# Optimization experiments

Measured on AMD Instinct MI355X. Metric: run time of the kernel, lower is better.

Reference implementation:

```python
import jax, jax.numpy as jnp
import numpy as np

N, C, T = 8, 256, 512
H, KQ, OUT = 8, 256, 256
EPS = 1e-5


def sym_linear(x, w, stride):
    # w: (2, out_dim); circulant-grouped expansion to (2T, out_dim), then x @ cp
    out_dim = w.shape[1]
    idx = (jnp.arange(out_dim)[None, :] - jnp.arange(T)[:, None] * stride) % out_dim  # (T, out_dim)
    cp = w[:, idx].transpose(1, 0, 2).reshape(2 * T, out_dim)  # cat of rolled copies
    return x @ cp


def ln2d(x, g, b):
    # LayerNorm over last two dims (T, 2T) with affine params (T, 2T)
    mu = jnp.mean(x, axis=(-2, -1), keepdims=True)
    var = jnp.mean(jnp.square(x - mu), axis=(-2, -1), keepdims=True)
    return (x - mu) / jnp.sqrt(var + EPS) * g + b


def setup_inputs() -> dict:
    key = jax.random.key(0)
    ks = jax.random.split(key, 16)
    stdv = 1.0 / np.sqrt(2 * T)
    u = lambda k, shape, s: jax.random.uniform(k, shape, jnp.float32, -s, s)
    return {
        "x": jax.random.normal(ks[0], (N, C, T), jnp.float32),
        "Wq": u(ks[1], (KQ, C), 1.0 / np.sqrt(C)),
        "Wk": u(ks[2], (KQ, C), 1.0 / np.sqrt(C)),
        "Wv": u(ks[3], (OUT, C), 1.0 / np.sqrt(C)),
        "m1w0": u(ks[4], (2, 2 * T), stdv),
        "m2w0": u(ks[5], (2, 2 * T), stdv),
        "m1w1": u(ks[6], (2, 2 * T), stdv),
        "m2w1": u(ks[7], (2, T), stdv),
        "ln1g0": 1.0 + 0.1 * jax.random.normal(ks[8], (T, 2 * T), jnp.float32),
        "ln1b0": 0.1 * jax.random.normal(ks[9], (T, 2 * T), jnp.float32),
        "ln2g0": 1.0 + 0.1 * jax.random.normal(ks[10], (T, 2 * T), jnp.float32),
        "ln2b0": 0.1 * jax.random.normal(ks[11], (T, 2 * T), jnp.float32),
        "ln1g1": 1.0 + 0.1 * jax.random.normal(ks[12], (T, 2 * T), jnp.float32),
        "ln1b1": 0.1 * jax.random.normal(ks[13], (T, 2 * T), jnp.float32),
    }


def reference(x, Wq, Wk, Wv, m1w0, m2w0, m1w1, m2w1,
              ln1g0, ln1b0, ln2g0, ln2b0, ln1g1, ln1b1):
    dk = KQ // H
    q = jnp.einsum('oc,nct->not', Wq, x).reshape(N, H, dk, T).transpose(0, 1, 3, 2)  # (N,H,T,dk)
    k = jnp.einsum('oc,nct->not', Wk, x).reshape(N, H, dk, T)                        # (N,H,dk,T)
    v = jnp.einsum('oc,nct->not', Wv, x).reshape(N, H, OUT // H, T).transpose(0, 1, 3, 2)  # (N,H,T,dv)

    scores = jnp.einsum('nhtd,nhds->nhts', q, k) / np.sqrt(dk)  # (N,H,T,T)
    ar = jnp.arange(T, dtype=jnp.float32)
    pd = jnp.abs(ar[None, :] - ar[:, None]) / (T - 1)  # (T,T)
    p = jnp.stack([scores, jnp.broadcast_to(pd, scores.shape)], axis=-1)  # (N,H,T,T,2)
    p = p.reshape(N, H, T, 2 * T)

    def transpose_pairs(z):
        return z.reshape(N, H, T, T, 2).transpose(0, 1, 3, 2, 4)

    # mix block 0 (intermediate)
    p = ln2d(sym_linear(p, m1w0, 2), ln1g0, ln1b0)
    p = jax.nn.gelu(transpose_pairs(p), approximate=False).reshape(N, H, T, 2 * T)
    p = ln2d(sym_linear(p, m2w0, 2), ln2g0, ln2b0)
    p = jax.nn.gelu(transpose_pairs(p), approximate=False).reshape(N, H, T, 2 * T)

    # mix block 1 (final)
    p = ln2d(sym_linear(p, m1w1, 2), ln1g1, ln1b1)
    p = jax.nn.gelu(transpose_pairs(p), approximate=False).reshape(N, H, T, 2 * T)
    p = sym_linear(p, m2w1, 1)           # (N,H,T,T), out_roll_stride = T // T * 1
    p = p.transpose(0, 1, 3, 2)

    attn = jax.nn.softmax(p, axis=-1)
    out = jnp.einsum('nhts,nhsd->nhtd', attn, v)  # (N,H,T,dv)
    return out.transpose(0, 1, 3, 2).reshape(N, OUT, T)
```

## Files before the change

### kernel.cpp

```cpp
#include <hip/hip_runtime.h>
#include <hip/hip_bf16.h>
#include <math.h>

#define CDIM 256
#define TDIM 512
#define T2   1024
#define NB   64
#define MTOT 524288.0f

typedef __bf16 bf16x8 __attribute__((ext_vector_type(8)));
typedef float  f32x4  __attribute__((ext_vector_type(4)));

__device__ __forceinline__ ushort f2bf(float f) {
  union { float f; unsigned u; } v; v.f = f;
  unsigned r = v.u + 0x7fffu + ((v.u >> 16) & 1u);
  return (ushort)(r >> 16);
}
__device__ __forceinline__ float bf2f(ushort h) {
  union { unsigned u; float f; } v; v.u = ((unsigned)h) << 16;
  return v.f;
}
__device__ __forceinline__ float gelu_exact(float x) {
  return 0.5f * x * (1.0f + erff(x * 0.7071067811865475f));
}

#define TO_LDS(p)  ((__attribute__((address_space(3))) void*)(unsigned)(uintptr_t)(p))
#define TO_GLB(p)  ((const __attribute__((address_space(1))) void*)(uintptr_t)(p))
#define GLOAD_LDS16(g, l) __builtin_amdgcn_global_load_lds(TO_GLB(g), TO_LDS(l), 16, 0, 0)

#define BAR()    asm volatile("s_barrier" ::: "memory")
#define WAITL()  asm volatile("s_waitcnt lgkmcnt(0)" ::: "memory")
#define WAITV4() asm volatile("s_waitcnt vmcnt(4)" ::: "memory")
#define WAITV0() asm volatile("s_waitcnt vmcnt(0)" ::: "memory")

__global__ __launch_bounds__(256)
void proj_kernel(const float* __restrict__ x, const float* __restrict__ Wq,
                 const float* __restrict__ Wk, const float* __restrict__ Wv,
                 ushort* __restrict__ qb, ushort* __restrict__ kb,
                 float* __restrict__ vp) {
  int t = blockIdx.x * 256 + threadIdx.x;
  int o = blockIdx.y;
  int n = blockIdx.z;
  const float* xn = x + (long)n * CDIM * TDIM;
  float aq = 0.f, ak = 0.f, av = 0.f;
  for (int c = 0; c < CDIM; ++c) {
    float xv = xn[c * TDIM + t];
    aq = fmaf(Wq[o * CDIM + c], xv, aq);
    ak = fmaf(Wk[o * CDIM + c], xv, ak);
    av = fmaf(Wv[o * CDIM + c], xv, av);
  }
  int h = o >> 5, d = o & 31;
  long bidx = (((long)(n * 8 + h) * 512) + t) * 32 + d;
  qb[bidx] = f2bf(aq);
  kb[bidx] = f2bf(ak);
  vp[((long)n * 256 + o) * TDIM + t] = av;
}

__global__ __launch_bounds__(256)
void prep_kernel(const float* __restrict__ m1w0, const float* __restrict__ m2w0,
                 const float* __restrict__ m1w1, const float* __restrict__ m2w1,
                 ushort* __restrict__ cpte0, ushort* __restrict__ cpto0,
                 ushort* __restrict__ cpt1, ushort* __restrict__ cpt2,
                 ushort* __restrict__ cpt3, ushort* __restrict__ pdb) {
  long i = (long)blockIdx.x * 256 + threadIdx.x;
  if (i < 524288) {
    int o = (int)(i >> 9), s = (int)(i & 511);
    int idx = (o - 2 * s) & 1023;
    cpte0[i] = f2bf(m1w0[idx]);
    cpto0[i] = f2bf(m1w0[1024 + idx]);
  } else if (i < 1572864) {
    long j = i - 524288;
    int o = (int)(j >> 10), kk = (int)(j & 1023);
    cpt1[j] = f2bf(m2w0[(kk & 1) * 1024 + ((o - 2 * (kk >> 1)) & 1023)]);
  } else if (i < 2621440) {
    long j = i - 1572864;
    int o = (int)(j >> 10), kk = (int)(j & 1023);
    cpt2[j] = f2bf(m1w1[(kk & 1) * 1024 + ((o - 2 * (kk >> 1)) & 1023)]);
  } else if (i < 3145728) {
    long j = i - 2621440;
    int o = (int)(j >> 10), kk = (int)(j & 1023);
    cpt3[j] = f2bf(m2w1[(kk & 1) * 512 + ((o - (kk >> 1)) & 511)]);
  } else if (i < 3407872) {
    long j = i - 3145728;
    int t = (int)(j >> 9), s = (int)(j & 511);
    pdb[j] = f2bf(fabsf((float)(s - t)) * (1.0f / 511.0f));
  }
}

__global__ __launch_bounds__(256)
void scores_kernel(const ushort* __restrict__ qb, const ushort* __restrict__ kb,
                   ushort* __restrict__ S) {
  int tb = blockIdx.x;
  int b  = blockIdx.y;
  int wv = threadIdx.x >> 6, lane = threadIdx.x & 63;
  int fr = lane & 15, fq = lane >> 4;
  int t0 = tb * 64 + wv * 16;
  bf16x8 af = *(const bf16x8*)(qb + ((long)b * 512 + t0 + fr) * 32 + fq * 8);
  const ushort* kbase = kb + (long)b * 512 * 32 + fr * 32 + fq * 8;
  ushort* Sb = S + ((long)b * 512 + t0 + fq * 4) * 512 + fr;
  f32x4 zz = {0.f, 0.f, 0.f, 0.f};
#pragma unroll 4
  for (int st = 0; st < 32; ++st) {
    bf16x8 bfv = *(const bf16x8*)(kbase + st * 512);
    f32x4 acc = __builtin_amdgcn_mfma_f32_16x16x32_bf16(af, bfv, zz, 0, 0, 0);
#pragma unroll
    for (int r = 0; r < 4; ++r)
      Sb[(long)r * 512 + st * 16] = f2bf(acc[r] * 0.17677669529663687f);
  }
}

#define LDS_BUF  65536
#define LDS_BOFF 32768

#define STAGE_A_(buf, h, kt) do { \
  const ushort* gA0_ = Ab + (long)((h)*128 +      sr0) * K + (kt)*64 + slog8; \
  const ushort* gA1_ = Ab + (long)((h)*128 + 64 + sr0) * K + (kt)*64 + slog8; \
  char* dA_ = ldsw + (size_t)(buf) * LDS_BUF + (h)*16384 + tid*16; \
  GLOAD_LDS16(gA0_, dA_); GLOAD_LDS16(gA1_, dA_ + 8192); } while(0)

#define STAGE_B_(buf, h, kt) do { \
  const ushort* gB0_ = Bb + (long)((h)*128 +      sr0) * K + (kt)*64 + slog8; \
  const ushort* gB1_ = Bb + (long)((h)*128 + 64 + sr0) * K + (kt)*64 + slog8; \
  char* dB_ = ldsw + (size_t)(buf) * LDS_BUF + LDS_BOFF + (h)*16384 + tid*16; \
  GLOAD_LDS16(gB0_, dB_); GLOAD_LDS16(gB1_, dB_ + 8192); } while(0)

#define LD_A_(buf, mh) do { \
  const char* aB_ = ldsc + (size_t)(buf) * LDS_BUF; \
  _Pragma("unroll") for (int mi = 0; mi < 4; ++mi) { \
    int ar_ = wm*128 + (mh)*64 + mi*16 + fr; \
    const char* rb_ = aB_ + ar_*128; int sw_ = (ar_&7)<<4; \
    af[mi][0] = *(const bf16x8*)(rb_ + ((fq*16) ^ sw_)); \
    af[mi][1] = *(const bf16x8*)(rb_ + ((64 + fq*16) ^ sw_)); \
  } } while(0)

#define LD_B_(dst, buf, nh) do { \
  const char* bB_ = ldsc + (size_t)(buf) * LDS_BUF + LDS_BOFF; \
  _Pragma("unroll") for (int ni = 0; ni < 2; ++ni) { \
    int br_ = wn*64 + (nh)*32 + ni*16 + fr; \
    const char* rb_ = bB_ + br_*128; int sw_ = (br_&7)<<4; \
    dst[ni][0] = *(const bf16x8*)(rb_ + ((fq*16) ^ sw_)); \
    dst[ni][1] = *(const bf16x8*)(rb_ + ((64 + fq*16) ^ sw_)); \
  } } while(0)

#define QUAD_(mh, nh, bfa) do { \
  __builtin_amdgcn_s_setprio(1); \
  _Pragma("unroll") for (int kk = 0; kk < 2; ++kk) \
  _Pragma("unroll") for (int mi = 0; mi < 4; ++mi) \
  _Pragma("unroll") for (int ni = 0; ni < 2; ++ni) \
    acc[(mh)*4+mi][(nh)*2+ni] = __builtin_amdgcn_mfma_f32_16x16x32_bf16( \
        af[mi][kk], bfa[ni][kk], acc[(mh)*4+mi][(nh)*2+ni], 0, 0, 0); \
  __builtin_amdgcn_s_setprio(0); } while(0)

template<int K, bool FINAL>
__global__ __launch_bounds__(512, 2)
void gemm256_kernel(const ushort* __restrict__ A, long aStride,
                    const ushort* __restrict__ BT, long bStride,
                    void* __restrict__ Out, int ncols, float* __restrict__ stats,
                    const float* __restrict__ Cadd) {
  __shared__ ushort lds[2][2][256 * 64];
  const int tid = threadIdx.x;
  const int bm = blockIdx.x, bn = blockIdx.y, b = blockIdx.z;
  constexpr int NKT2 = K >> 7;
  const ushort* Ab = A  + (long)b * aStride + (long)bm * 256 * K;
  const ushort* Bb = BT + (long)b * bStride + (long)bn * 256 * K;
  const int lane = tid & 63;
  const int fr = lane & 15, fq = lane >> 4;
  const int wid = tid >> 6, wm = wid >> 2, wn = wid & 3;
  const int sr0 = tid >> 3;
  const int slog8 = ((tid & 7) ^ (sr0 & 7)) * 8;
  const char* ldsc = (const char*)&lds[0][0][0];
  char*       ldsw = (char*)&lds[0][0][0];

  f32x4 acc[8][4] = {};
  bf16x8 af[4][2], bf0[2][2], bf1[2][2];

  STAGE_B_(0, 0, 0); STAGE_B_(0, 1, 0);
  STAGE_A_(0, 0, 0); STAGE_A_(0, 1, 0);
  STAGE_B_(1, 0, 1); STAGE_B_(1, 1, 1);
  WAITV4();
  BAR();

  for (int i = 0; i < NKT2; ++i) {
    const int t1 = 2 * i + 1, t2 = 2 * i + 2, t3 = 2 * i + 3;
    const bool st = (i < NKT2 - 1);
    LD_A_(0, 0); LD_B_(bf0, 0, 0);
    STAGE_A_(1, 0, t1);
    BAR(); WAITL(); QUAD_(0, 0, bf0); BAR();

    LD_B_(bf1, 0, 1);
    STAGE_A_(1, 1, t1);
    BAR(); WAITL(); QUAD_(0, 1, bf1); BAR();

    LD_A_(0, 1);
    if (st) STAGE_B_(0, 0, t2);
    BAR(); WAITL(); QUAD_(1, 1, bf1); BAR();

    if (st) { STAGE_B_(0, 1, t2); WAITV4(); } else { WAITV0(); }
    BAR(); QUAD_(1, 0, bf0); BAR();

    LD_A_(1, 0); LD_B_(bf0, 1, 0);
    if (st) STAGE_A_(0, 0, t2);
    BAR(); WAITL(); QUAD_(0, 0, bf0); BAR();

    LD_B_(bf1, 1, 1);
    if (st) STAGE_A_(0, 1, t2);
    BAR(); WAITL(); QUAD_(0, 1, bf1); BAR();

    LD_A_(1, 1);
    if (st) STAGE_B_(1, 0, t3);
    BAR(); WAITL(); QUAD_(1, 1, bf1); BAR();

    if (st) { STAGE_B_(1, 1, t3); WAITV4(); }
    BAR(); QUAD_(1, 0, bf0); BAR();
  }

  const int r0 = bm * 256 + wm * 128;
  const int c0 = bn * 256 + wn * 64;
  if (!FINAL) {
    ushort* Yb = (ushort*)Out + (long)b * 512 * ncols;
    float s1 = 0.f, s2 = 0.f;
#pragma unroll
    for (int mi = 0; mi < 8; ++mi)
#pragma unroll
      for (int ni = 0; ni < 4; ++ni)
#pragma unroll
        for (int r = 0; r < 4; ++r) {
          float v = acc[mi][ni][r];
          int row = r0 + mi * 16 + fq * 4 + r;
          int col = c0 + ni * 16 + fr;
          if (Cadd) v += Cadd[(long)row * ncols + col];
          s1 += v; s2 += v * v;
          Yb[(long)row * ncols + col] = f2bf(v);
        }
    __syncthreads();
    float* red = (float*)&lds[0][0][0];
    red[tid] = s1; red[tid + 512] = s2;
    __syncthreads();
    for (int off = 256; off > 0; off >>= 1) {
      if (tid < off) { red[tid] += red[tid + off]; red[512 + tid] += red[512 + tid + off]; }
      __syncthreads();
    }
    if (tid == 0) {
      atomicAdd(&stats[b * 2],     red[0]);
      atomicAdd(&stats[b * 2 + 1], red[512]);
    }
  } else {
    float* Lb = (float*)Out + (long)b * 512 * ncols;
#pragma unroll
    for (int mi = 0; mi < 8; ++mi)
#pragma unroll
      for (int ni = 0; ni < 4; ++ni)
#pragma unroll
        for (int r = 0; r < 4; ++r) {
          int row = r0 + mi * 16 + fq * 4 + r;
          int col = c0 + ni * 16 + fr;
          Lb[(long)row * ncols + col] = acc[mi][ni][r];
        }
  }
}

__global__ __launch_bounds__(256)
void apply_kernel(const ushort* __restrict__ Y, const float* __restrict__ stats,
                  const float* __restrict__ g, const float* __restrict__ bia,
                  ushort* __restrict__ P) {
  __shared__ ushort2 tile[32][33];
  int ti = blockIdx.x;
  int si = blockIdx.y;
  int b  = blockIdx.z;
  float mu  = stats[b * 2] * (1.0f / MTOT);
  float var = stats[b * 2 + 1] * (1.0f / MTOT) - mu * mu;
  float rstd = rsqrtf(var + 1e-5f);
  int tx = threadIdx.x & 31, ty = threadIdx.x >> 5;
  const ushort* Yb = Y + (long)b * 512 * 1024;
#pragma unroll
  for (int i = 0; i < 4; ++i) {
    int t  = ti * 32 + ty + i * 8;
    int sp = si * 32 + tx;
    ushort2 yv = *(const ushort2*)(Yb + (long)t * 1024 + 2 * sp);
    float2 gv = *(const float2*)(g   + (long)t * 1024 + 2 * sp);
    float2 bv = *(const float2*)(bia + (long)t * 1024 + 2 * sp);
    float y0 = (bf2f(yv.x) - mu) * rstd * gv.x + bv.x;
    float y1 = (bf2f(yv.y) - mu) * rstd * gv.y + bv.y;
    ushort2 o; o.x = f2bf(gelu_exact(y0)); o.y = f2bf(gelu_exact(y1));
    tile[ty + i * 8][tx] = o;
  }
  __syncthreads();
  ushort* Pb = P + (long)b * 512 * 1024;
#pragma unroll
  for (int i = 0; i < 4; ++i) {
    int srow = si * 32 + ty + i * 8;
    int tcol = ti * 32 + tx;
    ushort2 v = tile[tx][ty + i * 8];
    *(ushort2*)(Pb + (long)srow * 1024 + 2 * tcol) = v;
  }
}

__global__ __launch_bounds__(256)
void smax_av_kernel(const float* __restrict__ L, const float* __restrict__ vp,
                    float* __restrict__ out) {
  __shared__ float Lt[32][513];
  int bh = blockIdx.x;
  int at = blockIdx.y;
  int n = bh >> 3, h = bh & 7;
  int wv = threadIdx.x >> 6, lane = threadIdx.x & 63;
  for (int rr = 0; rr < 8; ++rr) {
    int row = wv * 8 + rr;
    int a = at * 32 + row;
    const float* Lr = L + ((long)bh * 512 + a) * 512;
    float e[8];
#pragma unroll
    for (int j = 0; j < 8; ++j) e[j] = Lr[j * 64 + lane];
    float m = e[0];
#pragma unroll
    for (int j = 1; j < 8; ++j) m = fmaxf(m, e[j]);
    for (int off = 32; off > 0; off >>= 1) m = fmaxf(m, __shfl_xor(m, off, 64));
    float s = 0.f;
#pragma unroll
    for (int j = 0; j < 8; ++j) { e[j] = expf(e[j] - m); s += e[j]; }
    for (int off = 32; off > 0; off >>= 1) s += __shfl_xor(s, off, 64);
    float inv = 1.0f / s;
#pragma unroll
    for (int j = 0; j < 8; ++j) Lt[row][j * 64 + lane] = e[j] * inv;
  }
  __syncthreads();
  int r  = threadIdx.x & 31;
  int d0 = (threadIdx.x >> 5) * 4;
  const float* vb = vp + ((long)n * 256 + h * 32) * 512;
  float a0 = 0.f, a1 = 0.f, a2 = 0.f, a3 = 0.f;
  for (int bc = 0; bc < 512; bc += 4) {
    float4 v0 = *(const float4*)(vb + (d0 + 0) * 512 + bc);
    float4 v1 = *(const float4*)(vb + (d0 + 1) * 512 + bc);
    float4 v2 = *(const float4*)(vb + (d0 + 2) * 512 + bc);
    float4 v3 = *(const float4*)(vb + (d0 + 3) * 512 + bc);
    float p0 = Lt[r][bc], p1 = Lt[r][bc + 1], p2 = Lt[r][bc + 2], p3 = Lt[r][bc + 3];
    a0 = fmaf(p0, v0.x, fmaf(p1, v0.y, fmaf(p2, v0.z, fmaf(p3, v0.w, a0))));
    a1 = fmaf(p0, v1.x, fmaf(p1, v1.y, fmaf(p2, v1.z, fmaf(p3, v1.w, a1))));
    a2 = fmaf(p0, v2.x, fmaf(p1, v2.y, fmaf(p2, v2.z, fmaf(p3, v2.w, a2))));
    a3 = fmaf(p0, v3.x, fmaf(p1, v3.y, fmaf(p2, v3.z, fmaf(p3, v3.w, a3))));
  }
  int a = at * 32 + r;
  float* ob = out + ((long)n * 256 + h * 32) * 512;
  ob[(d0 + 0) * 512 + a] = a0;
  ob[(d0 + 1) * 512 + a] = a1;
  ob[(d0 + 2) * 512 + a] = a2;
  ob[(d0 + 3) * 512 + a] = a3;
}

extern "C" void kernel_launch(void* const* d_in, const int* in_sizes, int n_in,
                              void* d_out, int out_size, void* d_ws, size_t ws_size,
                              hipStream_t stream) {
  const float* x     = (const float*)d_in[0];
  const float* Wq    = (const float*)d_in[1];
  const float* Wk    = (const float*)d_in[2];
  const float* Wv    = (const float*)d_in[3];
  const float* m1w0  = (const float*)d_in[4];
  const float* m2w0  = (const float*)d_in[5];
  const float* m1w1  = (const float*)d_in[6];
  const float* m2w1  = (const float*)d_in[7];
  const float* ln1g0 = (const float*)d_in[8];
  const float* ln1b0 = (const float*)d_in[9];
  const float* ln2g0 = (const float*)d_in[10];
  const float* ln2b0 = (const float*)d_in[11];
  const float* ln1g1 = (const float*)d_in[12];
  const float* ln1b1 = (const float*)d_in[13];

  char* w = (char*)d_ws;
  float*  vp     = (float*) (w + 0);
  ushort* qb     = (ushort*)(w + (4ull  << 20));
  ushort* kb     = (ushort*)(w + (6ull  << 20));
  float*  stats  = (float*) (w + (8ull  << 20));
  ushort* cpte0  = (ushort*)(w + (9ull  << 20));
  ushort* cpto0  = (ushort*)(w + (10ull << 20));
  ushort* cpt1   = (ushort*)(w + (11ull << 20));
  ushort* cpt2   = (ushort*)(w + (13ull << 20));
  ushort* cpt3   = (ushort*)(w + (15ull << 20));
  ushort* pdb    = (ushort*)(w + (16ull << 20));
  float*  pdpart = (float*) (w + (17ull << 20));
  ushort* bufA   = (ushort*)(w + (20ull << 20));
  ushort* bufB   = (ushort*)(w + (84ull << 20));
  ushort* S      = bufA;
  float*  L      = (float*)bufB;
  float*  outp   = (float*)d_out;

  hipMemsetAsync(stats, 0, 3 * NB * 2 * sizeof(float), stream);

  proj_kernel<<<dim3(2, 256, 8), 256, 0, stream>>>(x, Wq, Wk, Wv, qb, kb, vp);
  prep_kernel<<<13312, 256, 0, stream>>>(m1w0, m2w0, m1w1, m2w1,
                                         cpte0, cpto0, cpt1, cpt2, cpt3, pdb);
  scores_kernel<<<dim3(8, 64), 256, 0, stream>>>(qb, kb, S);
  gemm256_kernel<512, true><<<dim3(2, 4, 1), 512, 0, stream>>>(
      pdb, 0, cpto0, 0, pdpart, 1024, nullptr, nullptr);
  gemm256_kernel<512, false><<<dim3(2, 4, 64), 512, 0, stream>>>(
      S, 512L * 512, cpte0, 0, bufB, 1024, stats, pdpart);
  apply_kernel<<<dim3(16, 16, 64), 256, 0, stream>>>(bufB, stats, ln1g0, ln1b0, bufA);
  gemm256_kernel<1024, false><<<dim3(2, 4, 64), 512, 0, stream>>>(
      bufA, 512L * 1024, cpt1, 0, bufB, 1024, stats + 128, nullptr);
  apply_kernel<<<dim3(16, 16, 64), 256, 0, stream>>>(bufB, stats + 128, ln2g0, ln2b0, bufA);
  gemm256_kernel<1024, false><<<dim3(2, 4, 64), 512, 0, stream>>>(
      bufA, 512L * 1024, cpt2, 0, bufB, 1024, stats + 256, nullptr);
  apply_kernel<<<dim3(16, 16, 64), 256, 0, stream>>>(bufB, stats + 256, ln1g1, ln1b1, bufA);
  gemm256_kernel<1024, true><<<dim3(2, 2, 64), 512, 0, stream>>>(
      cpt3, 0, bufA, 512L * 1024, L, 512, nullptr, nullptr);
  smax_av_kernel<<<dim3(64, 16), 256, 0, stream>>>(L, vp, outp);
}
```

Before: 516.3 us.

## Pack LayerNorm affine params to bf16, widen apply loads, merge GEMM barrier phases

Adds a prep kernel that converts the three LayerNorm gamma/beta sets to interleaved bf16, reusing the qb, kb and cpte0 workspace regions after they are consumed. The apply kernel now covers a 32x64 tile with 8-element vector loads and 16-byte transposed stores, cutting fp32 parameter traffic and raising access width. The GEMM main loop merges pairs of quads under one barrier pair, halving barriers per k-step. Rounding gamma and beta to bf16 adds a small precision loss, and the buffer reuse relies on the qb, kb and cpte0 data no longer being needed.

```diff
diff --git a/kernel.cpp b/kernel.cpp
--- a/kernel.cpp
+++ b/kernel.cpp
@@ -10,6 +10,8 @@
 
 typedef __bf16 bf16x8 __attribute__((ext_vector_type(8)));
 typedef float  f32x4  __attribute__((ext_vector_type(4)));
+typedef ushort ushort8v __attribute__((ext_vector_type(8)));
+typedef ushort ushort4v __attribute__((ext_vector_type(4)));
 
 __device__ __forceinline__ ushort f2bf(float f) {
   union { float f; unsigned u; } v; v.f = f;
@@ -88,6 +90,24 @@
 }
 
 __global__ __launch_bounds__(256)
+void prep2_kernel(const float* __restrict__ g0, const float* __restrict__ b0,
+                  const float* __restrict__ g1, const float* __restrict__ b1,
+                  const float* __restrict__ g2, const float* __restrict__ b2,
+                  ushort* __restrict__ gbb0, ushort* __restrict__ gbb1,
+                  ushort* __restrict__ gbb2) {
+  long i = (long)blockIdx.x * 256 + threadIdx.x;
+  int set = (int)(i >> 18);
+  long j = i & 262143;
+  const float* g = set == 0 ? g0 : (set == 1 ? g1 : g2);
+  const float* b = set == 0 ? b0 : (set == 1 ? b1 : b2);
+  ushort* gbb    = set == 0 ? gbb0 : (set == 1 ? gbb1 : gbb2);
+  float2 gv = *(const float2*)(g + 2 * j);
+  float2 bv = *(const float2*)(b + 2 * j);
+  ushort4v o; o[0] = f2bf(gv.x); o[1] = f2bf(bv.x); o[2] = f2bf(gv.y); o[3] = f2bf(bv.y);
+  *(ushort4v*)(gbb + 4 * j) = o;
+}
+
+__global__ __launch_bounds__(256)
 void scores_kernel(const ushort* __restrict__ qb, const ushort* __restrict__ kb,
                    ushort* __restrict__ S) {
   int tb = blockIdx.x;
@@ -183,35 +203,26 @@
   for (int i = 0; i < NKT2; ++i) {
     const int t1 = 2 * i + 1, t2 = 2 * i + 2, t3 = 2 * i + 3;
     const bool st = (i < NKT2 - 1);
-    LD_A_(0, 0); LD_B_(bf0, 0, 0);
-    STAGE_A_(1, 0, t1);
-    BAR(); WAITL(); QUAD_(0, 0, bf0); BAR();
-
-    LD_B_(bf1, 0, 1);
-    STAGE_A_(1, 1, t1);
-    BAR(); WAITL(); QUAD_(0, 1, bf1); BAR();
-
+    LD_A_(0, 0); LD_B_(bf0, 0, 0); LD_B_(bf1, 0, 1);
+    STAGE_A_(1, 0, t1); STAGE_A_(1, 1, t1);
+    BAR(); WAITL();
+    QUAD_(0, 0, bf0); QUAD_(0, 1, bf1);
+    BAR();
     LD_A_(0, 1);
-    if (st) STAGE_B_(0, 0, t2);
-    BAR(); WAITL(); QUAD_(1, 1, bf1); BAR();
-
-    if (st) { STAGE_B_(0, 1, t2); WAITV4(); } else { WAITV0(); }
-    BAR(); QUAD_(1, 0, bf0); BAR();
-
-    LD_A_(1, 0); LD_B_(bf0, 1, 0);
-    if (st) STAGE_A_(0, 0, t2);
-    BAR(); WAITL(); QUAD_(0, 0, bf0); BAR();
-
-    LD_B_(bf1, 1, 1);
-    if (st) STAGE_A_(0, 1, t2);
-    BAR(); WAITL(); QUAD_(0, 1, bf1); BAR();
-
+    if (st) { STAGE_B_(0, 0, t2); STAGE_B_(0, 1, t2); WAITV4(); } else { WAITV0(); }
+    BAR(); WAITL();
+    QUAD_(1, 1, bf1); QUAD_(1, 0, bf0);
+    BAR();
+    LD_A_(1, 0); LD_B_(bf0, 1, 0); LD_B_(bf1, 1, 1);
+    if (st) { STAGE_A_(0, 0, t2); STAGE_A_(0, 1, t2); }
+    BAR(); WAITL();
+    QUAD_(0, 0, bf0); QUAD_(0, 1, bf1);
+    BAR();
     LD_A_(1, 1);
-    if (st) STAGE_B_(1, 0, t3);
-    BAR(); WAITL(); QUAD_(1, 1, bf1); BAR();
-
-    if (st) { STAGE_B_(1, 1, t3); WAITV4(); }
-    BAR(); QUAD_(1, 0, bf0); BAR();
+    if (st) { STAGE_B_(1, 0, t3); STAGE_B_(1, 1, t3); WAITV4(); }
+    BAR(); WAITL();
+    QUAD_(1, 1, bf1); QUAD_(1, 0, bf0);
+    BAR();
   }
 
   const int r0 = bm * 256 + wm * 128;
@@ -261,37 +272,52 @@
 
 __global__ __launch_bounds__(256)
 void apply_kernel(const ushort* __restrict__ Y, const float* __restrict__ stats,
-                  const float* __restrict__ g, const float* __restrict__ bia,
-                  ushort* __restrict__ P) {
-  __shared__ ushort2 tile[32][33];
+                  const ushort* __restrict__ gbb, ushort* __restrict__ P) {
+  __shared__ ushort2 tile[32][65];
   int ti = blockIdx.x;
   int si = blockIdx.y;
   int b  = blockIdx.z;
   float mu  = stats[b * 2] * (1.0f / MTOT);
   float var = stats[b * 2 + 1] * (1.0f / MTOT) - mu * mu;
   float rstd = rsqrtf(var + 1e-5f);
-  int tx = threadIdx.x & 31, ty = threadIdx.x >> 5;
   const ushort* Yb = Y + (long)b * 512 * 1024;
-#pragma unroll
-  for (int i = 0; i < 4; ++i) {
-    int t  = ti * 32 + ty + i * 8;
-    int sp = si * 32 + tx;
-    ushort2 yv = *(const ushort2*)(Yb + (long)t * 1024 + 2 * sp);
-    float2 gv = *(const float2*)(g   + (long)t * 1024 + 2 * sp);
-    float2 bv = *(const float2*)(bia + (long)t * 1024 + 2 * sp);
-    float y0 = (bf2f(yv.x) - mu) * rstd * gv.x + bv.x;
-    float y1 = (bf2f(yv.y) - mu) * rstd * gv.y + bv.y;
-    ushort2 o; o.x = f2bf(gelu_exact(y0)); o.y = f2bf(gelu_exact(y1));
-    tile[ty + i * 8][tx] = o;
+  int tr  = threadIdx.x >> 4;
+  int sp4 = (threadIdx.x & 15) * 4;
+#pragma unroll
+  for (int pass = 0; pass < 2; ++pass) {
+    int t  = ti * 32 + pass * 16 + tr;
+    int sp = si * 64 + sp4;
+    ushort8v yv  = *(const ushort8v*)(Yb + (long)t * 1024 + 2 * sp);
+    ushort8v gbA = *(const ushort8v*)(gbb + ((long)t * 512 + sp) * 4);
+    ushort8v gbB = *(const ushort8v*)(gbb + ((long)t * 512 + sp + 2) * 4);
+#pragma unroll
+    for (int j = 0; j < 4; ++j) {
+      int base = (j & 1) * 4;
+      ushort gg0 = (j < 2) ? gbA[base + 0] : gbB[base + 0];
+      ushort bb0 = (j < 2) ? gbA[base + 1] : gbB[base + 1];
+      ushort gg1 = (j < 2) ? gbA[base + 2] : gbB[base + 2];
+      ushort bb1 = (j < 2) ? gbA[base + 3] : gbB[base + 3];
+      float y0 = (bf2f(yv[2 * j])     - mu) * rstd * bf2f(gg0) + bf2f(bb0);
+      float y1 = (bf2f(yv[2 * j + 1]) - mu) * rstd * bf2f(gg1) + bf2f(bb1);
+      ushort2 o; o.x = f2bf(gelu_exact(y0)); o.y = f2bf(gelu_exact(y1));
+      tile[pass * 16 + tr][sp4 + j] = o;
+    }
   }
   __syncthreads();
   ushort* Pb = P + (long)b * 512 * 1024;
-#pragma unroll
-  for (int i = 0; i < 4; ++i) {
-    int srow = si * 32 + ty + i * 8;
-    int tcol = ti * 32 + tx;
-    ushort2 v = tile[tx][ty + i * 8];
-    *(ushort2*)(Pb + (long)srow * 1024 + 2 * tcol) = v;
+  int srow = threadIdx.x >> 3;
+  int t4   = (threadIdx.x & 7) * 4;
+#pragma unroll
+  for (int pass = 0; pass < 2; ++pass) {
+    int scol = pass * 32 + srow;
+    int s = si * 64 + scol;
+    ushort2 v0 = tile[t4 + 0][scol];
+    ushort2 v1 = tile[t4 + 1][scol];
+    ushort2 v2 = tile[t4 + 2][scol];
+    ushort2 v3 = tile[t4 + 3][scol];
+    int tcol0 = ti * 32 + t4;
+    ushort8v w2 = {v0.x, v0.y, v1.x, v1.y, v2.x, v2.y, v3.x, v3.y};
+    *(ushort8v*)(Pb + (long)s * 1024 + 2 * tcol0) = w2;
   }
 }
 
@@ -378,6 +404,9 @@
   float*  pdpart = (float*) (w + (17ull << 20));
   ushort* bufA   = (ushort*)(w + (20ull << 20));
   ushort* bufB   = (ushort*)(w + (84ull << 20));
+  ushort* gbb0   = qb;
+  ushort* gbb1   = kb;
+  ushort* gbb2   = cpte0;
   ushort* S      = bufA;
   float*  L      = (float*)bufB;
   float*  outp   = (float*)d_out;
@@ -392,13 +421,15 @@
       pdb, 0, cpto0, 0, pdpart, 1024, nullptr, nullptr);
   gemm256_kernel<512, false><<<dim3(2, 4, 64), 512, 0, stream>>>(
       S, 512L * 512, cpte0, 0, bufB, 1024, stats, pdpart);
-  apply_kernel<<<dim3(16, 16, 64), 256, 0, stream>>>(bufB, stats, ln1g0, ln1b0, bufA);
+  prep2_kernel<<<3072, 256, 0, stream>>>(ln1g0, ln1b0, ln2g0, ln2b0, ln1g1, ln1b1,
+                                         gbb0, gbb1, gbb2);
+  apply_kernel<<<dim3(16, 8, 64), 256, 0, stream>>>(bufB, stats, gbb0, bufA);
   gemm256_kernel<1024, false><<<dim3(2, 4, 64), 512, 0, stream>>>(
       bufA, 512L * 1024, cpt1, 0, bufB, 1024, stats + 128, nullptr);
-  apply_kernel<<<dim3(16, 16, 64), 256, 0, stream>>>(bufB, stats + 128, ln2g0, ln2b0, bufA);
+  apply_kernel<<<dim3(16, 8, 64), 256, 0, stream>>>(bufB, stats + 128, gbb1, bufA);
   gemm256_kernel<1024, false><<<dim3(2, 4, 64), 512, 0, stream>>>(
       bufA, 512L * 1024, cpt2, 0, bufB, 1024, stats + 256, nullptr);
-  apply_kernel<<<dim3(16, 16, 64), 256, 0, stream>>>(bufB, stats + 256, ln1g1, ln1b1, bufA);
+  apply_kernel<<<dim3(16, 8, 64), 256, 0, stream>>>(bufB, stats + 256, gbb2, bufA);
   gemm256_kernel<1024, true><<<dim3(2, 2, 64), 512, 0, stream>>>(
       cpt3, 0, bufA, 512L * 1024, L, 512, nullptr, nullptr);
   smax_av_kernel<<<dim3(64, 16), 256, 0, stream>>>(L, vp, outp);
```

Result: no change. 513.6 us (-0.5%).
